# Optimization experiments

Measured on AMD Instinct MI355X. Metric: run time of the kernel, lower is better.

The kernel has to match this reference:

```python
import jax, jax.numpy as jnp
import numpy as np

C = 256       # in_channels
IC = 128      # inter_channels = C // 2
G = 4         # num_group
D = IC // G   # per-group channels = 32
B, H, W_ = 4, 56, 56
EPS = 1e-5


def conv1x1(x, w, b=None):
    # x: (B,Cin,H,W), w: (Cout,Cin)
    y = jnp.einsum('bchw,oc->bohw', x, w)
    if b is not None:
        y = y + b[None, :, None, None]
    return y


def bn(x, scale, bias, mean, var):
    inv = scale / jnp.sqrt(var + EPS)
    return x * inv[None, :, None, None] + (bias - mean * inv)[None, :, None, None]


def setup_inputs():
    key = jax.random.key(0)
    ks = jax.random.split(key, 16)
    r = lambda k, shape, s=0.05: jax.random.normal(k, shape, jnp.float32) * s
    C4 = C // 4
    return {
        'x': jax.random.normal(ks[0], (B, C, H, W_), jnp.float32),
        'g_w': r(ks[1], (IC, C)), 'g_b': r(ks[2], (IC,)),
        'theta_w': r(ks[3], (IC, C)), 'theta_b': r(ks[4], (IC,)),
        'phi_w': r(ks[5], (IC, C)), 'phi_b': r(ks[6], (IC,)),
        'W_w': r(ks[7], (C, IC)), 'W_b': r(ks[8], (C,)),
        'bnW_scale': jnp.ones((C,)), 'bnW_bias': jnp.zeros((C,)),
        'bnW_mean': jnp.zeros((C,)), 'bnW_var': jnp.ones((C,)),
        'ff1_w': r(ks[9], (C4, C)),
        'ffbn1_scale': jnp.ones((C4,)), 'ffbn1_bias': jnp.zeros((C4,)),
        'ffbn1_mean': jnp.zeros((C4,)), 'ffbn1_var': jnp.ones((C4,)),
        'ff2_w': r(ks[10], (C4, C4, 3, 3)),
        'ffbn2_scale': jnp.ones((C4,)), 'ffbn2_bias': jnp.zeros((C4,)),
        'ffbn2_mean': jnp.zeros((C4,)), 'ffbn2_var': jnp.ones((C4,)),
        'ff3_w': r(ks[11], (C, C4)),
        'ffbn3_scale': jnp.ones((C,)), 'ffbn3_bias': jnp.zeros((C,)),
        'ffbn3_mean': jnp.zeros((C,)), 'ffbn3_var': jnp.ones((C,)),
    }


def reference(x, g_w, g_b, theta_w, theta_b, phi_w, phi_b, W_w, W_b,
              bnW_scale, bnW_bias, bnW_mean, bnW_var,
              ff1_w, ffbn1_scale, ffbn1_bias, ffbn1_mean, ffbn1_var,
              ff2_w, ffbn2_scale, ffbn2_bias, ffbn2_mean, ffbn2_var,
              ff3_w, ffbn3_scale, ffbn3_bias, ffbn3_mean, ffbn3_var):
    b, c, h, w = x.shape
    n = h * w
    # grouped non-local attention: channels split into G groups of D
    gx = conv1x1(x, g_w, g_b).reshape(b, G, D, n)       # (B,G,D,N)
    tx = conv1x1(x, theta_w, theta_b).reshape(b, G, D, n)
    px = conv1x1(x, phi_w, phi_b).reshape(b, G, D, n)
    f = jnp.einsum('bgdn,bgdm->bgnm', tx, px)           # (B,G,N,N) scores
    attn = jax.nn.softmax(f, axis=-1)                   # softmax over keys (torch dim=2 on (b,N,N))
    yy = jnp.einsum('bgnm,bgdm->bgdn', attn, gx)        # (B,G,D,N)
    y_out = yy.reshape(b, IC, h, w)
    W_y = bn(conv1x1(y_out, W_w, W_b), bnW_scale, bnW_bias, bnW_mean, bnW_var)
    z = jax.nn.relu(W_y + x)
    # FPNFFConv bottleneck FFN (BN in eval mode)
    o = jax.nn.relu(bn(conv1x1(z, ff1_w), ffbn1_scale, ffbn1_bias, ffbn1_mean, ffbn1_var))
    o = jax.lax.conv_general_dilated(o, ff2_w, (1, 1), 'SAME',
                                     dimension_numbers=('NCHW', 'OIHW', 'NCHW'))
    o = jax.nn.relu(bn(o, ffbn2_scale, ffbn2_bias, ffbn2_mean, ffbn2_var))
    o = bn(conv1x1(o, ff3_w), ffbn3_scale, ffbn3_bias, ffbn3_mean, ffbn3_var)
    return jax.nn.relu(o + z)
```

## Files before the change

kernel.cpp:

```cpp
#include <hip/hip_runtime.h>
#include <hip/hip_bf16.h>

#define NPIX 3136
#define BB 4
#define NSPLIT 5
#define LOG2E 1.4426950408889634f
#define ZLS 264

typedef unsigned short u16;
typedef __bf16 bf16x8 __attribute__((ext_vector_type(8)));
typedef float f32x4 __attribute__((ext_vector_type(4)));

__device__ __forceinline__ float b2f(u16 u) {
  union { unsigned u; float f; } c; c.u = ((unsigned)u) << 16; return c.f;
}
__device__ __forceinline__ u16 f2b(float f) {
  __hip_bfloat16 h = __float2bfloat16(f);
  return *reinterpret_cast<u16*>(&h);
}
__device__ __forceinline__ unsigned pk2(float a, float b) {
  return (unsigned)f2b(a) | ((unsigned)f2b(b) << 16);
}
__device__ __forceinline__ f32x4 mfma(bf16x8 a, bf16x8 b, f32x4 c) {
  return __builtin_amdgcn_mfma_f32_16x16x32_bf16(a, b, c, 0, 0, 0);
}
__device__ __forceinline__ float fast_exp2(float x) {
#if __has_builtin(__builtin_amdgcn_exp2f)
  return __builtin_amdgcn_exp2f(x);
#else
  float r; asm("v_exp_f32 %0, %1" : "=v"(r) : "v"(x)); return r;
#endif
}

template<int NSTEP, int NOT>
__device__ __forceinline__ void mf_gemm2(const u16* __restrict__ A0,
                                         const u16* __restrict__ A1,
                                         const u16* __restrict__ Brow, int sB,
                                         int lq, f32x4* acc) {
#pragma unroll
  for (int s = 0; s < NSTEP; ++s) {
    bf16x8 bf[NOT];
#pragma unroll
    for (int ot = 0; ot < NOT; ++ot)
      bf[ot] = *(const bf16x8*)(Brow + (size_t)ot * 16 * sB + s * 32 + lq * 8);
    bf16x8 a0 = *(const bf16x8*)(A0 + s * 32 + lq * 8);
    bf16x8 a1 = *(const bf16x8*)(A1 + s * 32 + lq * 8);
#pragma unroll
    for (int ot = 0; ot < NOT; ++ot) {
      acc[ot] = mfma(a0, bf[ot], acc[ot]);
      acc[NOT + ot] = mfma(a1, bf[ot], acc[NOT + ot]);
    }
  }
}

__global__ __launch_bounds__(256) void prep_w(
    const float* __restrict__ gw, const float* __restrict__ tw,
    const float* __restrict__ pw, const float* __restrict__ Ww,
    const float* __restrict__ f1w, const float* __restrict__ f2w,
    const float* __restrict__ f3w,
    u16* __restrict__ gwb, u16* __restrict__ twb, u16* __restrict__ pwb,
    u16* __restrict__ Wwb, u16* __restrict__ f1b, u16* __restrict__ f3b,
    u16* __restrict__ f2p) {
  for (int i = blockIdx.x * 256 + threadIdx.x; i < 200704; i += gridDim.x * 256) {
    int j = i;
    if (j < 32768) { gwb[j] = f2b(gw[j]); continue; } j -= 32768;
    if (j < 32768) { twb[j] = f2b(tw[j] * LOG2E); continue; } j -= 32768;
    if (j < 32768) { pwb[j] = f2b(pw[j]); continue; } j -= 32768;
    if (j < 32768) { Wwb[j] = f2b(Ww[j]); continue; } j -= 32768;
    if (j < 16384) { f1b[j] = f2b(f1w[j]); continue; } j -= 16384;
    if (j < 16384) { f3b[j] = f2b(f3w[j]); continue; } j -= 16384;
    int t = j >> 12, rem = j & 4095, co = rem >> 6, ci = rem & 63;
    f2p[j] = f2b(f2w[(co * 64 + ci) * 9 + t]);
  }
}

__global__ __launch_bounds__(256) void prep_x(const float* __restrict__ x,
                                              u16* __restrict__ xt) {
  __shared__ u16 sT[64 * 65];
  const int b = blockIdx.z, c0 = blockIdx.y * 64, n0 = blockIdx.x * 64;
  const int t = threadIdx.x;
#pragma unroll
  for (int cc = 0; cc < 4; ++cc) {
    int c = cc * 16 + (t >> 4), n4 = (t & 15) * 4;
    float4 v = *(const float4*)(x + ((size_t)(b * 256 + c0 + c)) * NPIX + n0 + n4);
    sT[c * 65 + n4 + 0] = f2b(v.x);
    sT[c * 65 + n4 + 1] = f2b(v.y);
    sT[c * 65 + n4 + 2] = f2b(v.z);
    sT[c * 65 + n4 + 3] = f2b(v.w);
  }
  __syncthreads();
#pragma unroll
  for (int nn = 0; nn < 4; ++nn) {
    int n = nn * 16 + (t >> 4), c4 = (t & 15) * 4;
    uint2 s;
    s.x = (unsigned)sT[(c4 + 0) * 65 + n] | ((unsigned)sT[(c4 + 1) * 65 + n] << 16);
    s.y = (unsigned)sT[(c4 + 2) * 65 + n] | ((unsigned)sT[(c4 + 3) * 65 + n] << 16);
    *(uint2*)(xt + ((size_t)b * NPIX + n0 + n) * 256 + c0 + c4) = s;
  }
}

__global__ __launch_bounds__(256) void proj_kernel(
    const u16* __restrict__ xt,
    const u16* __restrict__ gwb, const u16* __restrict__ twb, const u16* __restrict__ pwb,
    const float* __restrict__ gb, const float* __restrict__ tb, const float* __restrict__ pb,
    u16* __restrict__ gx, u16* __restrict__ Tq, u16* __restrict__ Pk) {
  const int b = blockIdx.z, oc = blockIdx.y, nb = blockIdx.x * 128;
  const int sec = oc >> 1, rbase = (oc & 1) * 64;
  const u16* wsel = sec == 0 ? gwb : (sec == 1 ? twb : pwb);
  const float* bsel = sec == 0 ? gb : (sec == 1 ? tb : pb);
  const int wv = threadIdx.x >> 6, lane = threadIdx.x & 63;
  const int lr = lane & 15, lq = lane >> 4;
  const int nrow0 = nb + wv * 32, nrow1 = nrow0 + 16;
  const int r0 = nrow0 + lr < NPIX ? nrow0 + lr : NPIX - 1;
  const int r1 = nrow1 + lr < NPIX ? nrow1 + lr : NPIX - 1;
  f32x4 acc[8] = {};
  mf_gemm2<8, 4>(xt + ((size_t)b * NPIX + r0) * 256,
                 xt + ((size_t)b * NPIX + r1) * 256,
                 wsel + (size_t)(rbase + lr) * 256, 256, lq, acc);
#pragma unroll
  for (int t = 0; t < 2; ++t) {
    const int qn = (t ? nrow1 : nrow0) + lq * 4;
    if (qn >= NPIX) continue;
#pragma unroll
    for (int ot = 0; ot < 4; ++ot) {
      const f32x4 a = acc[t * 4 + ot];
      const int o = rbase + ot * 16 + lr;
      float bias = bsel[o];
      if (sec == 1) bias *= LOG2E;
      if (sec == 0) {
        uint2 s;
        s.x = pk2(a[0] + bias, a[1] + bias);
        s.y = pk2(a[2] + bias, a[3] + bias);
        *(uint2*)(gx + ((size_t)b * 128 + o) * NPIX + qn) = s;
      } else {
        const int g = o >> 5, dl = o & 31;
        u16* dst = sec == 1 ? Tq : Pk;
        size_t base = (size_t)(b * 4 + g) * NPIX;
#pragma unroll
        for (int r = 0; r < 4; ++r)
          dst[(base + qn + r) * 32 + dl] = f2b(a[r] + bias);
      }
    }
  }
}

__global__ __launch_bounds__(256) void attn_kernel(
    const u16* __restrict__ Tq, const u16* __restrict__ Pk,
    const u16* __restrict__ gx, u16* __restrict__ OPb, float* __restrict__ LP) {
  __shared__ __align__(16) u16 Plds[4][32][40];
  const int bid = blockIdx.x;
  const int ks = bid / 400, rem = bid % 400;
  const int bg = rem / 25, qblk = rem % 25;
  const int b = bg >> 2, g = bg & 3;
  const int wave = threadIdx.x >> 6, lane = threadIdx.x & 63;
  const int lr = lane & 15, lq = lane >> 4;
  const int qbase = qblk * 128 + wave * 32;
  const int kc0 = ((ks * 98) / NSPLIT) * 32;
  const int kc1 = (((ks + 1) * 98) / NSPLIT) * 32;
  const u16* Qp = Tq + (size_t)bg * NPIX * 32;
  const u16* Kp = Pk + (size_t)bg * NPIX * 32;
  const u16* Vp = gx + ((size_t)b * 128 + g * 32) * NPIX;

  bf16x8 qf[2];
#pragma unroll
  for (int qi = 0; qi < 2; ++qi) {
    int row = qbase + qi * 16 + lr;
    row = row < NPIX ? row : NPIX - 1;
    qf[qi] = *(const bf16x8*)(Qp + (size_t)row * 32 + lq * 8);
  }
  const f32x4 z4 = {0.f, 0.f, 0.f, 0.f};
  f32x4 O[2][2], Lf[2];
#pragma unroll
  for (int qi = 0; qi < 2; ++qi) { O[qi][0] = z4; O[qi][1] = z4; Lf[qi] = z4; }
  bf16x8 onef;
#pragma unroll
  for (int j = 0; j < 8; ++j) onef[j] = (__bf16)1.0f;

#pragma unroll 1
  for (int kc = kc0; kc < kc1; kc += 32) {
    bf16x8 kf0 = *(const bf16x8*)(Kp + (size_t)(kc + lr) * 32 + lq * 8);
    bf16x8 kf1 = *(const bf16x8*)(Kp + (size_t)(kc + 16 + lr) * 32 + lq * 8);
    f32x4 St[2][2];
    St[0][0] = mfma(kf0, qf[0], z4);
    St[0][1] = mfma(kf0, qf[1], z4);
    St[1][0] = mfma(kf1, qf[0], z4);
    St[1][1] = mfma(kf1, qf[1], z4);
#pragma unroll
    for (int kt = 0; kt < 2; ++kt)
#pragma unroll
      for (int qi = 0; qi < 2; ++qi) {
        const f32x4 s = St[kt][qi];
        unsigned e0 = __builtin_bit_cast(unsigned, fast_exp2(s[0]));
        unsigned e1 = __builtin_bit_cast(unsigned, fast_exp2(s[1]));
        unsigned e2 = __builtin_bit_cast(unsigned, fast_exp2(s[2]));
        unsigned e3 = __builtin_bit_cast(unsigned, fast_exp2(s[3]));
        uint2 pk;
        pk.x = __builtin_amdgcn_perm(e1, e0, 0x07060302u);
        pk.y = __builtin_amdgcn_perm(e3, e2, 0x07060302u);
        *(uint2*)(&Plds[wave][qi * 16 + lr][kt * 16 + lq * 4]) = pk;
      }
    bf16x8 pf0 = *(const bf16x8*)(&Plds[wave][lr][lq * 8]);
    bf16x8 pf1 = *(const bf16x8*)(&Plds[wave][16 + lr][lq * 8]);
    bf16x8 vf0 = *(const bf16x8*)(Vp + (size_t)lr * NPIX + kc + lq * 8);
    bf16x8 vf1 = *(const bf16x8*)(Vp + (size_t)(16 + lr) * NPIX + kc + lq * 8);
    O[0][0] = mfma(pf0, vf0, O[0][0]);
    O[0][1] = mfma(pf0, vf1, O[0][1]);
    O[1][0] = mfma(pf1, vf0, O[1][0]);
    O[1][1] = mfma(pf1, vf1, O[1][1]);
    Lf[0] = mfma(pf0, onef, Lf[0]);
    Lf[1] = mfma(pf1, onef, Lf[1]);
  }
  const size_t sbase = (size_t)(ks * 16 + bg) * NPIX;
#pragma unroll
  for (int qi = 0; qi < 2; ++qi) {
#pragma unroll
    for (int r = 0; r < 4; ++r) {
      int qrow = qbase + qi * 16 + lq * 4 + r;
      if (qrow < NPIX) {
        size_t ob = (sbase + qrow) * 32;
        OPb[ob + lr] = f2b(O[qi][0][r]);
        OPb[ob + 16 + lr] = f2b(O[qi][1][r]);
        if (lr == 0) LP[sbase + qrow] = Lf[qi][r];
      }
    }
  }
}

__global__ __launch_bounds__(512) void wz_kernel(
    const u16* __restrict__ OPb, const float* __restrict__ LP,
    const u16* __restrict__ Wwb, const float* __restrict__ Wb,
    const float* __restrict__ sc, const float* __restrict__ bi,
    const float* __restrict__ mu, const float* __restrict__ var,
    const float* __restrict__ x,
    const u16* __restrict__ f1b, const float* __restrict__ s1,
    const float* __restrict__ b1, const float* __restrict__ m1,
    const float* __restrict__ v1,
    u16* __restrict__ zt, u16* __restrict__ o1t) {
  __shared__ float Ls[4][32];
  __shared__ __align__(16) u16 zl[32 * ZLS];
  const int b = blockIdx.y, nb = blockIdx.x * 32;
  const int tid = threadIdx.x;
  if (tid < 128) {
    int g = tid >> 5, row = tid & 31;
    float l = 0.f;
#pragma unroll
    for (int ks = 0; ks < NSPLIT; ++ks)
      l += LP[(size_t)(ks * 16 + b * 4 + g) * NPIX + nb + row];
    Ls[g][row] = 1.0f / l;
  }
  __syncthreads();
  const int wave = tid >> 6, lane = tid & 63;
  const int lr = lane & 15, lq = lane >> 4;
  const int oc = wave & 3, tt = wave >> 2;
  const int nrow = nb + tt * 16;
  f32x4 acc[4][4] = {};
#pragma unroll
  for (int g = 0; g < 4; ++g) {
    bf16x8 bf[4];
#pragma unroll
    for (int ot = 0; ot < 4; ++ot)
      bf[ot] = *(const bf16x8*)(Wwb + (size_t)(oc * 64 + ot * 16 + lr) * 128 + g * 32 + lq * 8);
#pragma unroll
    for (int ks = 0; ks < NSPLIT; ++ks) {
      bf16x8 af = *(const bf16x8*)(OPb +
          ((size_t)(ks * 16 + b * 4 + g) * NPIX + nrow + lr) * 32 + lq * 8);
#pragma unroll
      for (int ot = 0; ot < 4; ++ot)
        acc[g][ot] = mfma(af, bf[ot], acc[g][ot]);
    }
  }
#pragma unroll
  for (int ot = 0; ot < 4; ++ot) {
    const int o = oc * 64 + ot * 16 + lr;
    float inv = sc[o] * rsqrtf(var[o] + 1e-5f);
    float off = bi[o] - mu[o] * inv + Wb[o] * inv;
    const int qn = nrow + lq * 4;
    float4 xr = *(const float4*)(x + ((size_t)b * 256 + o) * NPIX + qn);
    float xv[4] = {xr.x, xr.y, xr.z, xr.w};
#pragma unroll
    for (int r = 0; r < 4; ++r) {
      int row = tt * 16 + lq * 4 + r;
      float y = acc[0][ot][r] * Ls[0][row] + acc[1][ot][r] * Ls[1][row] +
                acc[2][ot][r] * Ls[2][row] + acc[3][ot][r] * Ls[3][row];
      float v = fmaxf(y * inv + off + xv[r], 0.f);
      u16 vb = f2b(v);
      zt[((size_t)b * NPIX + qn + r) * 256 + o] = vb;
      zl[row * ZLS + o] = vb;
    }
  }
  __syncthreads();
  const int oc2 = wave & 3, tt2 = wave >> 2;
  f32x4 a1 = {0.f, 0.f, 0.f, 0.f};
  const u16* Bw = f1b + (size_t)(oc2 * 16 + lr) * 256;
#pragma unroll
  for (int s = 0; s < 8; ++s) {
    bf16x8 a0 = *(const bf16x8*)(&zl[(tt2 * 16 + lr) * ZLS + s * 32 + lq * 8]);
    bf16x8 bw = *(const bf16x8*)(Bw + s * 32 + lq * 8);
    a1 = mfma(a0, bw, a1);
  }
  const int o1 = oc2 * 16 + lr;
  float inv1 = s1[o1] * rsqrtf(v1[o1] + 1e-5f);
  float off1 = b1[o1] - m1[o1] * inv1;
  const int pr = nb + tt2 * 16 + lq * 4;
#pragma unroll
  for (int r = 0; r < 4; ++r) {
    float v = fmaxf(a1[r] * inv1 + off1, 0.f);
    o1t[((size_t)b * NPIX + pr + r) * 64 + o1] = f2b(v);
  }
}

__global__ __launch_bounds__(512) void ff23_kernel(
    const u16* __restrict__ o1t, const u16* __restrict__ f2p,
    const float* __restrict__ s2, const float* __restrict__ b2,
    const float* __restrict__ m2, const float* __restrict__ v2,
    const u16* __restrict__ f3b,
    const float* __restrict__ s3, const float* __restrict__ b3,
    const float* __restrict__ m3, const float* __restrict__ v3,
    const u16* __restrict__ zt, float* __restrict__ out) {
  __shared__ __align__(16) u16 o2l[128 * 72];
  const int b = blockIdx.y, nb = blockIdx.x * 128;
  const int tid = threadIdx.x;
  const int wave = tid >> 6, lane = tid & 63;
  const int lr = lane & 15, lq = lane >> 4;
  {
    const int n0 = nb + wave * 16 + lr;
    const int n0c = n0 < NPIX ? n0 : NPIX - 1;
    const int h0 = n0c / 56, w0 = n0c % 56;
    f32x4 acc2[4] = {};
#pragma unroll
    for (int t = 0; t < 9; ++t) {
      const int dh = t / 3 - 1, dw = t % 3 - 1;
      const bool v0 = n0 < NPIX && (h0 + dh) >= 0 && (h0 + dh) < 56 &&
                      (w0 + dw) >= 0 && (w0 + dw) < 56;
      const u16* A0 = o1t + ((size_t)b * NPIX + n0c + dh * 56 + dw) * 64;
      const u16* Br = f2p + (size_t)t * 4096 + (size_t)lr * 64;
#pragma unroll
      for (int k2 = 0; k2 < 2; ++k2) {
        bf16x8 a0 = {};
        if (v0) a0 = *(const bf16x8*)(A0 + k2 * 32 + lq * 8);
#pragma unroll
        for (int ot = 0; ot < 4; ++ot) {
          bf16x8 bf = *(const bf16x8*)(Br + (size_t)ot * 16 * 64 + k2 * 32 + lq * 8);
          acc2[ot] = mfma(a0, bf, acc2[ot]);
        }
      }
    }
#pragma unroll
    for (int ot = 0; ot < 4; ++ot) {
      const int o = ot * 16 + lr;
      float inv = s2[o] * rsqrtf(v2[o] + 1e-5f);
      float off = b2[o] - m2[o] * inv;
#pragma unroll
      for (int r = 0; r < 4; ++r) {
        float v = fmaxf(acc2[ot][r] * inv + off, 0.f);
        o2l[(wave * 16 + lq * 4 + r) * 72 + o] = f2b(v);
      }
    }
  }
  __syncthreads();
  const int oc3 = wave & 3, tt3 = wave >> 2;
  bf16x8 bf3[4][2];
#pragma unroll
  for (int ot = 0; ot < 4; ++ot)
#pragma unroll
    for (int s = 0; s < 2; ++s)
      bf3[ot][s] = *(const bf16x8*)(f3b +
          (size_t)(oc3 * 64 + ot * 16 + lr) * 64 + s * 32 + lq * 8);
#pragma unroll
  for (int rt = 0; rt < 4; ++rt) {
    const int lrow = tt3 * 64 + rt * 16;
    bf16x8 a0 = *(const bf16x8*)(&o2l[(lrow + lr) * 72 + lq * 8]);
    bf16x8 a1 = *(const bf16x8*)(&o2l[(lrow + lr) * 72 + 32 + lq * 8]);
    f32x4 acc3[4] = {};
#pragma unroll
    for (int ot = 0; ot < 4; ++ot) {
      acc3[ot] = mfma(a0, bf3[ot][0], acc3[ot]);
      acc3[ot] = mfma(a1, bf3[ot][1], acc3[ot]);
    }
    const int qn = nb + lrow + lq * 4;
    if (qn < NPIX) {
#pragma unroll
      for (int ot = 0; ot < 4; ++ot) {
        const int o = oc3 * 64 + ot * 16 + lr;
        float inv = s3[o] * rsqrtf(v3[o] + 1e-5f);
        float off = b3[o] - m3[o] * inv;
        float4 sv4;
        float* sv = (float*)&sv4;
#pragma unroll
        for (int r = 0; r < 4; ++r) {
          float zres = b2f(zt[((size_t)b * NPIX + qn + r) * 256 + o]);
          sv[r] = fmaxf(acc3[ot][r] * inv + off + zres, 0.f);
        }
        *(float4*)(out + ((size_t)b * 256 + o) * NPIX + qn) = sv4;
      }
    }
  }
}

extern "C" void kernel_launch(void* const* d_in, const int* in_sizes, int n_in,
                              void* d_out, int out_size, void* d_ws, size_t ws_size,
                              hipStream_t stream) {
  const float* x    = (const float*)d_in[0];
  const float* gw   = (const float*)d_in[1];
  const float* gb   = (const float*)d_in[2];
  const float* tw   = (const float*)d_in[3];
  const float* tb   = (const float*)d_in[4];
  const float* pw   = (const float*)d_in[5];
  const float* pb   = (const float*)d_in[6];
  const float* Ww   = (const float*)d_in[7];
  const float* Wb   = (const float*)d_in[8];
  const float* bnWs = (const float*)d_in[9];
  const float* bnWb = (const float*)d_in[10];
  const float* bnWm = (const float*)d_in[11];
  const float* bnWv = (const float*)d_in[12];
  const float* f1w  = (const float*)d_in[13];
  const float* b1s  = (const float*)d_in[14];
  const float* b1b  = (const float*)d_in[15];
  const float* b1m  = (const float*)d_in[16];
  const float* b1v  = (const float*)d_in[17];
  const float* f2w  = (const float*)d_in[18];
  const float* b2s  = (const float*)d_in[19];
  const float* b2b  = (const float*)d_in[20];
  const float* b2m  = (const float*)d_in[21];
  const float* b2v  = (const float*)d_in[22];
  const float* f3w  = (const float*)d_in[23];
  const float* b3s  = (const float*)d_in[24];
  const float* b3b  = (const float*)d_in[25];
  const float* b3m  = (const float*)d_in[26];
  const float* b3v  = (const float*)d_in[27];
  float* out = (float*)d_out;

  u16* p = (u16*)d_ws;
  u16* xt  = p; p += (size_t)BB * NPIX * 256;
  u16* gwb = p; p += 128 * 256;
  u16* twb = p; p += 128 * 256;
  u16* pwb = p; p += 128 * 256;
  u16* Wwb = p; p += 256 * 128;
  u16* f1b = p; p += 64 * 256;
  u16* f3b = p; p += 256 * 64;
  u16* f2p = p; p += 9 * 64 * 64;
  u16* Tq  = p; p += (size_t)16 * NPIX * 32;
  u16* Pk  = p; p += (size_t)16 * NPIX * 32;
  u16* gx  = p; p += (size_t)BB * 128 * NPIX;
  u16* OPb = p; p += (size_t)7 * 16 * NPIX * 32;
  float* LP = (float*)p; p += (size_t)7 * 16 * NPIX * 2;
  u16* zt  = p; p += (size_t)BB * NPIX * 256;
  u16* o1t = p; p += (size_t)BB * NPIX * 64;
  u16* o2t = p; p += (size_t)BB * NPIX * 64;
  (void)o2t;

  prep_w<<<dim3(196), 256, 0, stream>>>(gw, tw, pw, Ww, f1w, f2w, f3w,
                                        gwb, twb, pwb, Wwb, f1b, f3b, f2p);
  prep_x<<<dim3(49, 4, BB), 256, 0, stream>>>(x, xt);
  proj_kernel<<<dim3(25, 6, BB), 256, 0, stream>>>(xt, gwb, twb, pwb, gb, tb, pb,
                                                   gx, Tq, Pk);
  attn_kernel<<<dim3(NSPLIT * 400), 256, 0, stream>>>(Tq, Pk, gx, OPb, LP);
  wz_kernel<<<dim3(98, BB), 512, 0, stream>>>(OPb, LP, Wwb, Wb,
                                              bnWs, bnWb, bnWm, bnWv, x,
                                              f1b, b1s, b1b, b1m, b1v,
                                              zt, o1t);
  ff23_kernel<<<dim3(25, BB), 512, 0, stream>>>(o1t, f2p, b2s, b2b, b2m, b2v,
                                                f3b, b3s, b3b, b3m, b3v,
                                                zt, out);
}
```

Measured before the change: 251.3 us.

## Shrink ff23 pixel tile to 32 and split output channels across waves

The fused 3x3-conv plus 1x1-conv kernel now processes 32 pixels per block instead of 128, launching 98x4 blocks instead of 25x4. Each wave computes one 16-channel slice of the 3x3 conv output for 16 pixels, and one 64-channel slice of the final 1x1 conv, which drops the tail-bounds checks because 3136 divides evenly by 32. The aim is to fill more compute units, since 100 blocks underuse the GPU. The cost is that each block reloads the 3x3 and 1x1 weights, and each wave does less MFMA work per load.

```diff
diff --git a/kernel.cpp b/kernel.cpp
--- a/kernel.cpp
+++ b/kernel.cpp
@@ -6,6 +6,7 @@
 #define NSPLIT 5
 #define LOG2E 1.4426950408889634f
 #define ZLS 264
+#define O2S 72
 
 typedef unsigned short u16;
 typedef __bf16 bf16x8 __attribute__((ext_vector_type(8)));
@@ -317,83 +318,63 @@
     const float* __restrict__ s3, const float* __restrict__ b3,
     const float* __restrict__ m3, const float* __restrict__ v3,
     const u16* __restrict__ zt, float* __restrict__ out) {
-  __shared__ __align__(16) u16 o2l[128 * 72];
-  const int b = blockIdx.y, nb = blockIdx.x * 128;
+  __shared__ __align__(16) u16 o2l[32 * O2S];
+  const int b = blockIdx.y, nb = blockIdx.x * 32;
   const int tid = threadIdx.x;
   const int wave = tid >> 6, lane = tid & 63;
   const int lr = lane & 15, lq = lane >> 4;
   {
-    const int n0 = nb + wave * 16 + lr;
-    const int n0c = n0 < NPIX ? n0 : NPIX - 1;
-    const int h0 = n0c / 56, w0 = n0c % 56;
-    f32x4 acc2[4] = {};
+    const int rt = wave >> 2, oq = wave & 3;
+    const int n0 = nb + rt * 16 + lr;
+    const int h0 = n0 / 56, w0 = n0 % 56;
+    f32x4 acc2 = {0.f, 0.f, 0.f, 0.f};
 #pragma unroll
     for (int t = 0; t < 9; ++t) {
       const int dh = t / 3 - 1, dw = t % 3 - 1;
-      const bool v0 = n0 < NPIX && (h0 + dh) >= 0 && (h0 + dh) < 56 &&
+      const bool v0 = (h0 + dh) >= 0 && (h0 + dh) < 56 &&
                       (w0 + dw) >= 0 && (w0 + dw) < 56;
-      const u16* A0 = o1t + ((size_t)b * NPIX + n0c + dh * 56 + dw) * 64;
-      const u16* Br = f2p + (size_t)t * 4096 + (size_t)lr * 64;
+      const u16* A0 = o1t + ((size_t)b * NPIX + n0 + dh * 56 + dw) * 64;
+      const u16* Br = f2p + (size_t)t * 4096 + (size_t)(oq * 16 + lr) * 64;
 #pragma unroll
       for (int k2 = 0; k2 < 2; ++k2) {
         bf16x8 a0 = {};
         if (v0) a0 = *(const bf16x8*)(A0 + k2 * 32 + lq * 8);
-#pragma unroll
-        for (int ot = 0; ot < 4; ++ot) {
-          bf16x8 bf = *(const bf16x8*)(Br + (size_t)ot * 16 * 64 + k2 * 32 + lq * 8);
-          acc2[ot] = mfma(a0, bf, acc2[ot]);
-        }
+        bf16x8 bf = *(const bf16x8*)(Br + k2 * 32 + lq * 8);
+        acc2 = mfma(a0, bf, acc2);
       }
     }
-#pragma unroll
-    for (int ot = 0; ot < 4; ++ot) {
-      const int o = ot * 16 + lr;
-      float inv = s2[o] * rsqrtf(v2[o] + 1e-5f);
-      float off = b2[o] - m2[o] * inv;
-#pragma unroll
-      for (int r = 0; r < 4; ++r) {
-        float v = fmaxf(acc2[ot][r] * inv + off, 0.f);
-        o2l[(wave * 16 + lq * 4 + r) * 72 + o] = f2b(v);
-      }
+    const int o = oq * 16 + lr;
+    float inv = s2[o] * rsqrtf(v2[o] + 1e-5f);
+    float off = b2[o] - m2[o] * inv;
+#pragma unroll
+    for (int r = 0; r < 4; ++r) {
+      float v = fmaxf(acc2[r] * inv + off, 0.f);
+      o2l[(rt * 16 + lq * 4 + r) * O2S + o] = f2b(v);
     }
   }
   __syncthreads();
-  const int oc3 = wave & 3, tt3 = wave >> 2;
-  bf16x8 bf3[4][2];
-#pragma unroll
-  for (int ot = 0; ot < 4; ++ot)
-#pragma unroll
-    for (int s = 0; s < 2; ++s)
-      bf3[ot][s] = *(const bf16x8*)(f3b +
-          (size_t)(oc3 * 64 + ot * 16 + lr) * 64 + s * 32 + lq * 8);
-#pragma unroll
-  for (int rt = 0; rt < 4; ++rt) {
-    const int lrow = tt3 * 64 + rt * 16;
-    bf16x8 a0 = *(const bf16x8*)(&o2l[(lrow + lr) * 72 + lq * 8]);
-    bf16x8 a1 = *(const bf16x8*)(&o2l[(lrow + lr) * 72 + 32 + lq * 8]);
-    f32x4 acc3[4] = {};
-#pragma unroll
-    for (int ot = 0; ot < 4; ++ot) {
-      acc3[ot] = mfma(a0, bf3[ot][0], acc3[ot]);
-      acc3[ot] = mfma(a1, bf3[ot][1], acc3[ot]);
-    }
-    const int qn = nb + lrow + lq * 4;
-    if (qn < NPIX) {
-#pragma unroll
-      for (int ot = 0; ot < 4; ++ot) {
-        const int o = oc3 * 64 + ot * 16 + lr;
-        float inv = s3[o] * rsqrtf(v3[o] + 1e-5f);
-        float off = b3[o] - m3[o] * inv;
-        float4 sv4;
-        float* sv = (float*)&sv4;
-#pragma unroll
-        for (int r = 0; r < 4; ++r) {
-          float zres = b2f(zt[((size_t)b * NPIX + qn + r) * 256 + o]);
-          sv[r] = fmaxf(acc3[ot][r] * inv + off + zres, 0.f);
-        }
-        *(float4*)(out + ((size_t)b * 256 + o) * NPIX + qn) = sv4;
-      }
-    }
+  const int rt2 = wave >> 2, ocq = wave & 3;
+  bf16x8 a0 = *(const bf16x8*)(&o2l[(rt2 * 16 + lr) * O2S + lq * 8]);
+  bf16x8 a1 = *(const bf16x8*)(&o2l[(rt2 * 16 + lr) * O2S + 32 + lq * 8]);
+  const int qn = nb + rt2 * 16 + lq * 4;
+#pragma unroll
+  for (int ot = 0; ot < 4; ++ot) {
+    const int o = ocq * 64 + ot * 16 + lr;
+    bf16x8 b0 = *(const bf16x8*)(f3b + (size_t)o * 64 + lq * 8);
+    bf16x8 b1f = *(const bf16x8*)(f3b + (size_t)o * 64 + 32 + lq * 8);
+    f32x4 acc3 = {0.f, 0.f, 0.f, 0.f};
+    acc3 = mfma(a0, b0, acc3);
+    acc3 = mfma(a1, b1f, acc3);
+    float inv = s3[o] * rsqrtf(v3[o] + 1e-5f);
+    float off = b3[o] - m3[o] * inv;
+    float4 sv4;
+    float* sv = (float*)&sv4;
+#pragma unroll
+    for (int r = 0; r < 4; ++r) {
+      float zres = b2f(zt[((size_t)b * NPIX + qn + r) * 256 + o]);
+      sv[r] = fmaxf(acc3[r] * inv + off + zres, 0.f);
+    }
+    *(float4*)(out + ((size_t)b * 256 + o) * NPIX + qn) = sv4;
   }
 }
 
@@ -459,7 +440,7 @@
                                               bnWs, bnWb, bnWm, bnWv, x,
                                               f1b, b1s, b1b, b1m, b1v,
                                               zt, o1t);
-  ff23_kernel<<<dim3(25, BB), 512, 0, stream>>>(o1t, f2p, b2s, b2b, b2m, b2v,
+  ff23_kernel<<<dim3(98, BB), 512, 0, stream>>>(o1t, f2p, b2s, b2b, b2m, b2v,
                                                 f3b, b3s, b3b, b3m, b3v,
                                                 zt, out);
 }
```

After: 249.0 us. About the same (-0.9%).
